# Optimization experiments

Hardware: AMD Instinct MI355X
Metric: run time of the kernel (lower is better)

## Reference

```python
import jax, jax.numpy as jnp
import numpy as np

D, N_T, N, N_H = 8, 2048, 64, 8
STD_E = 0.02
STD_Q = 0.02


def setup_inputs() -> dict:
    key = jax.random.key(0)
    k1, k2, k3 = jax.random.split(key, 3)
    r_prime = jax.random.normal(k1, (D, N_T, N), dtype=jnp.float32)
    Q = jax.random.normal(k2, (N_H, N, N), dtype=jnp.float32) * STD_Q
    E = jax.random.normal(k3, (N_H, N, N), dtype=jnp.float32) * STD_E
    return {"r_prime": r_prime, "Q": Q, "E": E}


def reference(r_prime, Q, E):
    # r_prime: (b=d, t=n_t, i=n); Q, E: (h, i, j)
    n_t = r_prime.shape[1]
    # Omega[b,h,t,u] = sum_ij r'[b,t,i] Q[h,i,j] r'[b,u,j]
    Qr = jnp.einsum('hij,buj->bhui', Q, r_prime)          # (b, h, u, i)
    Omega = jnp.einsum('bti,bhui->bhtu', r_prime, Qr)     # (b, h, t, u)
    # causal lower-triangular mask (t >= u)
    mask = jnp.tril(jnp.ones((n_t, n_t), dtype=r_prime.dtype))
    Omega = Omega * mask  # broadcast over (b, h)
    # r[b,t,i] = sum_{h,u,j} Omega[b,h,t,u] E[h,i,j] r'[b,u,j]
    Er = jnp.einsum('hij,buj->bhui', E, r_prime)          # (b, h, u, i)
    r = jnp.einsum('bhtu,bhui->bti', Omega, Er)           # (b, t, i)
    return r
```

## Files before the change

### kernel.cpp

```cpp
#include <hip/hip_runtime.h>

#define D_B 8
#define N_T 2048
#define NN  64
#define N_H 8
#define N_C 32
#define NP  72

typedef __bf16 bf16;
typedef bf16 bf16x8 __attribute__((ext_vector_type(8)));
typedef bf16 bf16x4 __attribute__((ext_vector_type(4)));
typedef float f32x4 __attribute__((ext_vector_type(4)));

static __device__ __forceinline__ f32x4 mfma16(bf16x8 a, bf16x8 b, f32x4 c) {
    return __builtin_amdgcn_mfma_f32_16x16x32_bf16(a, b, c, 0, 0, 0);
}

static __device__ __forceinline__ bf16x8 ldcvt8(const float* p) {
    const f32x4 v0 = *(const f32x4*)p;
    const f32x4 v1 = *(const f32x4*)(p + 4);
    bf16x8 r;
#pragma unroll
    for (int k = 0; k < 4; k++) { r[k] = (bf16)v0[k]; r[4 + k] = (bf16)v1[k]; }
    return r;
}

__global__ __launch_bounds__(256, 3) void k_dg(
    const float* __restrict__ rp, const float* __restrict__ Qm,
    const float* __restrict__ Em,
    bf16* __restrict__ dGq, bf16* __restrict__ Rbf,
    bf16* __restrict__ Qrd, bf16* __restrict__ Erd)
{
    __shared__ bf16 Rl[64 * NP];
    __shared__ bf16 Ql[64 * NP];
    __shared__ bf16 El[64 * NP];
    __shared__ bf16 QT[64 * NP];
    __shared__ bf16 ET[64 * NP];
    const int b = blockIdx.x, c = blockIdx.y, qt = blockIdx.z;
    const int tid = threadIdx.x;
    const int w = tid >> 6, l = tid & 63, q = l >> 4, l16 = l & 15;
    const int row = tid >> 2, col = (tid & 3) * 16;

    {
        const float* src = rp + ((size_t)b * N_T + c * 64 + row) * NN + col;
        const bf16x8 v0 = ldcvt8(src), v1 = ldcvt8(src + 8);
        *(bf16x8*)&Rl[row * NP + col] = v0;
        *(bf16x8*)&Rl[row * NP + col + 8] = v1;
        if (qt == 0) {
            bf16* d = Rbf + ((size_t)b * N_T + c * 64 + row) * NN + col;
            *(bf16x8*)d = v0;
            *(bf16x8*)(d + 8) = v1;
        }
    }
    __syncthreads();
    const bf16x8 a0 = *(const bf16x8*)&Rl[(w * 16 + l16) * NP + q * 8];
    const bf16x8 a1 = *(const bf16x8*)&Rl[(w * 16 + l16) * NP + 32 + q * 8];

    f32x4 dacc[4];
#pragma unroll
    for (int ns = 0; ns < 4; ns++) { f32x4 z = {0.f, 0.f, 0.f, 0.f}; dacc[ns] = z; }

    for (int hh = 0; hh < 2; hh++) {
        const int h = qt * 2 + hh;
        {
            const float* qs = Qm + (size_t)h * 4096 + row * 64 + col;
            const float* es = Em + (size_t)h * 4096 + row * 64 + col;
            *(bf16x8*)&Ql[row * NP + col]     = ldcvt8(qs);
            *(bf16x8*)&Ql[row * NP + col + 8] = ldcvt8(qs + 8);
            *(bf16x8*)&El[row * NP + col]     = ldcvt8(es);
            *(bf16x8*)&El[row * NP + col + 8] = ldcvt8(es + 8);
        }
        __syncthreads();
        const size_t tb = (((size_t)(b * N_C + c)) * N_H + h) * 4096;
#pragma unroll
        for (int ns = 0; ns < 4; ns++) {
            bf16x8 b0 = *(const bf16x8*)&Ql[(ns * 16 + l16) * NP + q * 8];
            bf16x8 b1 = *(const bf16x8*)&Ql[(ns * 16 + l16) * NP + 32 + q * 8];
            f32x4 z = {0.f, 0.f, 0.f, 0.f};
            f32x4 s = mfma16(a0, b0, z);
            s = mfma16(a1, b1, s);
            bf16x4 p;
#pragma unroll
            for (int r = 0; r < 4; r++) p[r] = (bf16)s[r];
#pragma unroll
            for (int r = 0; r < 4; r++)
                Qrd[tb + (w * 16 + q * 4 + r) * 64 + ns * 16 + l16] = p[r];
            *(bf16x4*)&QT[(ns * 16 + l16) * NP + w * 16 + q * 4] = p;
            b0 = *(const bf16x8*)&El[(ns * 16 + l16) * NP + q * 8];
            b1 = *(const bf16x8*)&El[(ns * 16 + l16) * NP + 32 + q * 8];
            f32x4 s2 = mfma16(a0, b0, z);
            s2 = mfma16(a1, b1, s2);
#pragma unroll
            for (int r = 0; r < 4; r++) p[r] = (bf16)s2[r];
            *(bf16x4*)&ET[(ns * 16 + l16) * NP + w * 16 + q * 4] = p;
        }
        __syncthreads();
        {
            const bf16x8 qa0 = *(const bf16x8*)&QT[(w * 16 + l16) * NP + q * 8];
            const bf16x8 qa1 = *(const bf16x8*)&QT[(w * 16 + l16) * NP + 32 + q * 8];
#pragma unroll
            for (int ns = 0; ns < 4; ns++) {
                const bf16x8 e0 = *(const bf16x8*)&ET[(ns * 16 + l16) * NP + q * 8];
                const bf16x8 e1 = *(const bf16x8*)&ET[(ns * 16 + l16) * NP + 32 + q * 8];
                dacc[ns] = mfma16(qa0, e0, dacc[ns]);
                dacc[ns] = mfma16(qa1, e1, dacc[ns]);
            }
        }
        {
            const bf16x8 v0 = *(const bf16x8*)&ET[row * NP + col];
            const bf16x8 v1 = *(const bf16x8*)&ET[row * NP + col + 8];
            bf16* d = Erd + tb + row * 64 + col;
            *(bf16x8*)d = v0;
            *(bf16x8*)(d + 8) = v1;
        }
        __syncthreads();
    }
#pragma unroll
    for (int ns = 0; ns < 4; ns++) {
        bf16x4 p;
#pragma unroll
        for (int r = 0; r < 4; r++) p[r] = (bf16)dacc[ns][r];
        *(bf16x4*)&QT[(ns * 16 + l16) * NP + w * 16 + q * 4] = p;
    }
    __syncthreads();
    {
        bf16* dst = dGq + (((size_t)(b * N_C + c)) * 4 + qt) * 4096 + row * 64 + col;
        *(bf16x8*)dst       = *(const bf16x8*)&QT[row * NP + col];
        *(bf16x8*)(dst + 8) = *(const bf16x8*)&QT[row * NP + col + 8];
    }
}

__global__ __launch_bounds__(512, 2) void k_out(
    const bf16* __restrict__ dGq, const bf16* __restrict__ Rbf,
    const bf16* __restrict__ Qrd, const bf16* __restrict__ Erd,
    float* __restrict__ out)
{
    __shared__ bf16 Gb[64 * NP];
    __shared__ char sm2[8 * 16 * NP * 2];
    bf16* Sl = (bf16*)sm2;
    float* Ob = (float*)sm2;
    const int b = blockIdx.x, c = blockIdx.y;
    const int tid = threadIdx.x;
    const int w = tid >> 6, l = tid & 63, q = l >> 4, l16 = l & 15;
    const int g = w >> 2, s = w & 3;

    {
        float run[8];
#pragma unroll
        for (int k = 0; k < 8; k++) run[k] = 0.f;
        const bf16* base = dGq + (size_t)b * N_C * 4 * 4096 + tid * 8;
        for (int cp = 0; cp < c; cp++) {
#pragma unroll
            for (int qt = 0; qt < 4; qt++) {
                const bf16x8 v = *(const bf16x8*)(base + ((size_t)(cp * 4 + qt)) * 4096);
#pragma unroll
                for (int k = 0; k < 8; k++) run[k] += (float)v[k];
            }
        }
        bf16x8 o;
#pragma unroll
        for (int k = 0; k < 8; k++) o[k] = (bf16)run[k];
        *(bf16x8*)&Gb[(tid >> 3) * NP + (tid & 7) * 8] = o;
    }
    __syncthreads();

    const bf16x8 ra0 = *(const bf16x8*)&Rbf[((size_t)b * N_T + c * 64 + s * 16 + l16) * NN + q * 8];
    const bf16x8 ra1 = *(const bf16x8*)&Rbf[((size_t)b * N_T + c * 64 + s * 16 + l16) * NN + 32 + q * 8];

    bf16* Sw = Sl + w * 16 * NP;
    f32x4 acc[4];
#pragma unroll
    for (int ns = 0; ns < 4; ns++) { f32x4 z = {0.f, 0.f, 0.f, 0.f}; acc[ns] = z; }

    for (int hh = 0; hh < 4; hh++) {
        const int h = g * 4 + hh;
        const bf16* Qh = Qrd + (((size_t)(b * N_C + c)) * N_H + h) * 4096;
        const bf16* Eh = Erd + (((size_t)(b * N_C + c)) * N_H + h) * 4096;
#pragma unroll
        for (int ns = 0; ns < 4; ns++) {
            const bf16x8 b0 = *(const bf16x8*)&Qh[(ns * 16 + l16) * 64 + q * 8];
            const bf16x8 b1 = *(const bf16x8*)&Qh[(ns * 16 + l16) * 64 + 32 + q * 8];
            f32x4 z = {0.f, 0.f, 0.f, 0.f};
            f32x4 sv = mfma16(ra0, b0, z);
            sv = mfma16(ra1, b1, sv);
            const int u_loc = ns * 16 + l16;
#pragma unroll
            for (int r = 0; r < 4; r++) {
                const int t_loc = s * 16 + q * 4 + r;
                Sw[(q * 4 + r) * NP + u_loc] = (u_loc <= t_loc) ? (bf16)sv[r] : (bf16)0.f;
            }
        }
        const bf16x8 sa0 = *(const bf16x8*)&Sw[l16 * NP + q * 8];
        const bf16x8 sa1 = *(const bf16x8*)&Sw[l16 * NP + 32 + q * 8];
#pragma unroll
        for (int ns = 0; ns < 4; ns++) {
            const bf16x8 e0 = *(const bf16x8*)&Eh[(ns * 16 + l16) * 64 + q * 8];
            const bf16x8 e1 = *(const bf16x8*)&Eh[(ns * 16 + l16) * 64 + 32 + q * 8];
            acc[ns] = mfma16(sa0, e0, acc[ns]);
            acc[ns] = mfma16(sa1, e1, acc[ns]);
        }
    }
    if (g == 1) {
#pragma unroll
        for (int ns = 0; ns < 4; ns++) {
            const bf16x8 g0 = *(const bf16x8*)&Gb[(ns * 16 + l16) * NP + q * 8];
            const bf16x8 g1 = *(const bf16x8*)&Gb[(ns * 16 + l16) * NP + 32 + q * 8];
            acc[ns] = mfma16(ra0, g0, acc[ns]);
            acc[ns] = mfma16(ra1, g1, acc[ns]);
        }
    }
    __syncthreads();
    if (g == 0) {
#pragma unroll
        for (int ns = 0; ns < 4; ns++)
#pragma unroll
            for (int r = 0; r < 4; r++)
                Ob[(s * 16 + q * 4 + r) * 65 + ns * 16 + l16] = acc[ns][r];
    }
    __syncthreads();
    if (g == 1) {
        const int t0 = c * 64;
#pragma unroll
        for (int ns = 0; ns < 4; ns++)
#pragma unroll
            for (int r = 0; r < 4; r++) {
                const float sum = acc[ns][r] + Ob[(s * 16 + q * 4 + r) * 65 + ns * 16 + l16];
                out[((size_t)b * N_T + t0 + s * 16 + q * 4 + r) * NN + ns * 16 + l16] = sum;
            }
    }
}

extern "C" void kernel_launch(void* const* d_in, const int* in_sizes, int n_in,
                              void* d_out, int out_size, void* d_ws, size_t ws_size,
                              hipStream_t stream) {
    const float* rp = (const float*)d_in[0];
    const float* Qm = (const float*)d_in[1];
    const float* Em = (const float*)d_in[2];
    float* out = (float*)d_out;

    bf16* dGq = (bf16*)d_ws;
    bf16* Rbf = dGq + (size_t)D_B * N_C * 4 * 4096;
    bf16* Qrd = Rbf + (size_t)D_B * N_T * NN;
    bf16* Erd = Qrd + (size_t)D_B * N_C * N_H * 4096;

    k_dg<<<dim3(D_B, N_C, 4), 256, 0, stream>>>(rp, Qm, Em, dGq, Rbf, Qrd, Erd);
    k_out<<<dim3(D_B, N_C), 512, 0, stream>>>(dGq, Rbf, Qrd, Erd, out);
}
```

Before: 110.7 us.

## Pre-fold per-chunk dG partials and split output kernel into causal halves

After: 107.6 us. 1.03x faster.

```diff
diff --git a/kernel.cpp b/kernel.cpp
--- a/kernel.cpp
+++ b/kernel.cpp
@@ -130,44 +130,67 @@
     }
 }
 
-__global__ __launch_bounds__(512, 2) void k_out(
-    const bf16* __restrict__ dGq, const bf16* __restrict__ Rbf,
+__global__ __launch_bounds__(256, 4) void k_fold(const bf16* __restrict__ dGq,
+                                                 bf16* __restrict__ dG8)
+{
+    const int b = blockIdx.x, c = blockIdx.y;
+    const size_t base = ((size_t)(b * N_C + c)) * 4 * 4096 + threadIdx.x * 16;
+    float s[16];
+#pragma unroll
+    for (int k = 0; k < 16; k++) s[k] = 0.f;
+#pragma unroll
+    for (int qt = 0; qt < 4; qt++) {
+        const bf16x8 v0 = *(const bf16x8*)(dGq + base + (size_t)qt * 4096);
+        const bf16x8 v1 = *(const bf16x8*)(dGq + base + (size_t)qt * 4096 + 8);
+#pragma unroll
+        for (int k = 0; k < 8; k++) { s[k] += (float)v0[k]; s[8 + k] += (float)v1[k]; }
+    }
+    bf16x8 o0, o1;
+#pragma unroll
+    for (int k = 0; k < 8; k++) { o0[k] = (bf16)s[k]; o1[k] = (bf16)s[8 + k]; }
+    bf16* dst = dG8 + (size_t)(b * N_C + c) * 4096 + threadIdx.x * 16;
+    *(bf16x8*)dst = o0;
+    *(bf16x8*)(dst + 8) = o1;
+}
+
+__global__ __launch_bounds__(256, 4) void k_out(
+    const bf16* __restrict__ dG8, const bf16* __restrict__ Rbf,
     const bf16* __restrict__ Qrd, const bf16* __restrict__ Erd,
     float* __restrict__ out)
 {
     __shared__ bf16 Gb[64 * NP];
-    __shared__ char sm2[8 * 16 * NP * 2];
-    bf16* Sl = (bf16*)sm2;
-    float* Ob = (float*)sm2;
-    const int b = blockIdx.x, c = blockIdx.y;
+    __shared__ bf16 Sl[4 * 16 * NP];
+    __shared__ float Ob[32 * 65];
+    const int b = blockIdx.x, c = blockIdx.y, half = blockIdx.z;
     const int tid = threadIdx.x;
     const int w = tid >> 6, l = tid & 63, q = l >> 4, l16 = l & 15;
-    const int g = w >> 2, s = w & 3;
+    const int s = w & 1, g = w >> 1;
 
     {
-        float run[8];
-#pragma unroll
-        for (int k = 0; k < 8; k++) run[k] = 0.f;
-        const bf16* base = dGq + (size_t)b * N_C * 4 * 4096 + tid * 8;
+        float run[16];
+#pragma unroll
+        for (int k = 0; k < 16; k++) run[k] = 0.f;
+        const bf16* base = dG8 + (size_t)b * N_C * 4096 + tid * 16;
         for (int cp = 0; cp < c; cp++) {
-#pragma unroll
-            for (int qt = 0; qt < 4; qt++) {
-                const bf16x8 v = *(const bf16x8*)(base + ((size_t)(cp * 4 + qt)) * 4096);
-#pragma unroll
-                for (int k = 0; k < 8; k++) run[k] += (float)v[k];
-            }
-        }
-        bf16x8 o;
-#pragma unroll
-        for (int k = 0; k < 8; k++) o[k] = (bf16)run[k];
-        *(bf16x8*)&Gb[(tid >> 3) * NP + (tid & 7) * 8] = o;
-    }
-    __syncthreads();
-
-    const bf16x8 ra0 = *(const bf16x8*)&Rbf[((size_t)b * N_T + c * 64 + s * 16 + l16) * NN + q * 8];
-    const bf16x8 ra1 = *(const bf16x8*)&Rbf[((size_t)b * N_T + c * 64 + s * 16 + l16) * NN + 32 + q * 8];
+            const bf16x8 v0 = *(const bf16x8*)(base + (size_t)cp * 4096);
+            const bf16x8 v1 = *(const bf16x8*)(base + (size_t)cp * 4096 + 8);
+#pragma unroll
+            for (int k = 0; k < 8; k++) { run[k] += (float)v0[k]; run[8 + k] += (float)v1[k]; }
+        }
+        bf16x8 o0, o1;
+#pragma unroll
+        for (int k = 0; k < 8; k++) { o0[k] = (bf16)run[k]; o1[k] = (bf16)run[8 + k]; }
+        *(bf16x8*)&Gb[(tid >> 2) * NP + (tid & 3) * 16] = o0;
+        *(bf16x8*)&Gb[(tid >> 2) * NP + (tid & 3) * 16 + 8] = o1;
+    }
+    __syncthreads();
+
+    const int trow = c * 64 + half * 32 + s * 16 + l16;
+    const bf16x8 ra0 = *(const bf16x8*)&Rbf[((size_t)b * N_T + trow) * NN + q * 8];
+    const bf16x8 ra1 = *(const bf16x8*)&Rbf[((size_t)b * N_T + trow) * NN + 32 + q * 8];
 
     bf16* Sw = Sl + w * 16 * NP;
+    const int NU = half ? 4 : 2;
     f32x4 acc[4];
 #pragma unroll
     for (int ns = 0; ns < 4; ns++) { f32x4 z = {0.f, 0.f, 0.f, 0.f}; acc[ns] = z; }
@@ -176,28 +199,32 @@
         const int h = g * 4 + hh;
         const bf16* Qh = Qrd + (((size_t)(b * N_C + c)) * N_H + h) * 4096;
         const bf16* Eh = Erd + (((size_t)(b * N_C + c)) * N_H + h) * 4096;
-#pragma unroll
-        for (int ns = 0; ns < 4; ns++) {
-            const bf16x8 b0 = *(const bf16x8*)&Qh[(ns * 16 + l16) * 64 + q * 8];
-            const bf16x8 b1 = *(const bf16x8*)&Qh[(ns * 16 + l16) * 64 + 32 + q * 8];
+        for (int nu = 0; nu < NU; nu++) {
+            const bf16x8 b0 = *(const bf16x8*)&Qh[(nu * 16 + l16) * 64 + q * 8];
+            const bf16x8 b1 = *(const bf16x8*)&Qh[(nu * 16 + l16) * 64 + 32 + q * 8];
             f32x4 z = {0.f, 0.f, 0.f, 0.f};
             f32x4 sv = mfma16(ra0, b0, z);
             sv = mfma16(ra1, b1, sv);
-            const int u_loc = ns * 16 + l16;
+            const int u_loc = nu * 16 + l16;
 #pragma unroll
             for (int r = 0; r < 4; r++) {
-                const int t_loc = s * 16 + q * 4 + r;
+                const int t_loc = half * 32 + s * 16 + q * 4 + r;
                 Sw[(q * 4 + r) * NP + u_loc] = (u_loc <= t_loc) ? (bf16)sv[r] : (bf16)0.f;
             }
         }
         const bf16x8 sa0 = *(const bf16x8*)&Sw[l16 * NP + q * 8];
-        const bf16x8 sa1 = *(const bf16x8*)&Sw[l16 * NP + 32 + q * 8];
 #pragma unroll
         for (int ns = 0; ns < 4; ns++) {
             const bf16x8 e0 = *(const bf16x8*)&Eh[(ns * 16 + l16) * 64 + q * 8];
-            const bf16x8 e1 = *(const bf16x8*)&Eh[(ns * 16 + l16) * 64 + 32 + q * 8];
             acc[ns] = mfma16(sa0, e0, acc[ns]);
-            acc[ns] = mfma16(sa1, e1, acc[ns]);
+        }
+        if (half) {
+            const bf16x8 sa1 = *(const bf16x8*)&Sw[l16 * NP + 32 + q * 8];
+#pragma unroll
+            for (int ns = 0; ns < 4; ns++) {
+                const bf16x8 e1 = *(const bf16x8*)&Eh[(ns * 16 + l16) * 64 + 32 + q * 8];
+                acc[ns] = mfma16(sa1, e1, acc[ns]);
+            }
         }
     }
     if (g == 1) {
@@ -209,7 +236,6 @@
             acc[ns] = mfma16(ra1, g1, acc[ns]);
         }
     }
-    __syncthreads();
     if (g == 0) {
 #pragma unroll
         for (int ns = 0; ns < 4; ns++)
@@ -219,7 +245,7 @@
     }
     __syncthreads();
     if (g == 1) {
-        const int t0 = c * 64;
+        const int t0 = c * 64 + half * 32;
 #pragma unroll
         for (int ns = 0; ns < 4; ns++)
 #pragma unroll
@@ -242,7 +268,9 @@
     bf16* Rbf = dGq + (size_t)D_B * N_C * 4 * 4096;
     bf16* Qrd = Rbf + (size_t)D_B * N_T * NN;
     bf16* Erd = Qrd + (size_t)D_B * N_C * N_H * 4096;
+    bf16* dG8 = Erd + (size_t)D_B * N_C * N_H * 4096;
 
     k_dg<<<dim3(D_B, N_C, 4), 256, 0, stream>>>(rp, Qm, Em, dGq, Rbf, Qrd, Erd);
-    k_out<<<dim3(D_B, N_C), 512, 0, stream>>>(dGq, Rbf, Qrd, Erd, out);
-}
+    k_fold<<<dim3(D_B, N_C), 256, 0, stream>>>(dGq, dG8);
+    k_out<<<dim3(D_B, N_C, 2), 256, 0, stream>>>(dG8, Rbf, Qrd, Erd, out);
+}
```
